# Performance work log

Measured on AMD Instinct MI355X. Metric: run time of the kernel, lower is better.

The kernel has to match this reference:

```python
import jax, jax.numpy as jnp
import numpy as np

B, S, E, H = 4, 1024, 256, 8
D = E // H


def setup_inputs() -> dict:
    key = jax.random.key(0)
    ks = jax.random.split(key, 10)
    def lin(k, fin, fout):
        return jax.random.normal(k, (fin, fout), jnp.float32) / np.sqrt(fin)
    return {
        'x': jax.random.normal(ks[0], (B, S, E), jnp.float32),
        'Wq': lin(ks[1], E, E),
        'Wk': lin(ks[2], E, E),
        'Wv': lin(ks[3], E, E),
        'W_off1': lin(ks[4], E, E // 2),
        'b_off1': jnp.zeros((E // 2,), jnp.float32),
        'W_off2': lin(ks[5], E // 2, 2 * H),
        'b_off2': jnp.zeros((2 * H,), jnp.float32),
        'W_out': lin(ks[6], E, E),
        'b_out': jnp.zeros((E,), jnp.float32),
    }


def _forward(x, Wq, Wk, Wv, W_off1, b_off1, W_off2, b_off2, W_out, b_out):
    Bb, Ss, Ee = x.shape
    scale = 1.0 / np.sqrt(D)
    # offsets: (B,S,H,2) -- [...,0]=x-offset (col), [...,1]=y-offset (row)
    off = jax.nn.gelu(x @ W_off1 + b_off1, approximate=False) @ W_off2 + b_off2
    off = off.reshape(Bb, Ss, H, 2)
    q = (x @ Wq).reshape(Bb, Ss, H, D).transpose(0, 2, 1, 3)  # bhsd
    k = (x @ Wk).reshape(Bb, Ss, H, D).transpose(0, 2, 1, 3)
    v = (x @ Wv).reshape(Bb, Ss, H, D).transpose(0, 2, 1, 3)
    scores = jnp.einsum('bhid,bhjd->bhij', q, k) * scale  # (B,H,S,S)

    ox = off[..., 0].transpose(0, 2, 1)  # (B,H,S)
    oy = off[..., 1].transpose(0, 2, 1)
    cols = jnp.arange(Ss, dtype=x.dtype)
    xs = cols[None, None, None, :] + ox[..., None]          # (B,H,S,S) sample col
    ys = cols[None, None, :, None] + oy[..., None]          # (B,H,S,1) sample row

    x0 = jnp.floor(xs); x1 = x0 + 1.0
    y0 = jnp.floor(ys); y1 = y0 + 1.0
    wx = xs - x0  # (B,H,S,S)
    wy = ys - y0  # (B,H,S,1)
    lim = jnp.asarray(Ss - 1, x.dtype)

    def corner(yf, xf):
        # bilinear corner sample with zeros padding (align_corners=True)
        yc = jnp.clip(yf, 0, lim).astype(jnp.int32)
        xc = jnp.clip(xf, 0, lim).astype(jnp.int32)
        rows = jnp.take_along_axis(scores, jnp.broadcast_to(yc, scores.shape), axis=2)
        vals = jnp.take_along_axis(rows, jnp.broadcast_to(xc, rows.shape), axis=3)
        valid = (yf >= 0) & (yf <= lim) & (xf >= 0) & (xf <= lim)
        return jnp.where(valid, vals, jnp.zeros((), x.dtype))

    deformed = (corner(y0, x0) * (1 - wy) * (1 - wx)
                + corner(y0, x1) * (1 - wy) * wx
                + corner(y1, x0) * wy * (1 - wx)
                + corner(y1, x1) * wy * wx)

    attn = jax.nn.softmax(deformed, axis=-1)  # dropout is identity in eval
    out = jnp.einsum('bhij,bhjd->bhid', attn, v)
    out = out.transpose(0, 2, 1, 3).reshape(Bb, Ss, Ee)
    return out @ W_out + b_out


def reference(x, Wq, Wk, Wv, W_off1, b_off1, W_off2, b_off2, W_out, b_out):
    return _forward(x, Wq, Wk, Wv, W_off1, b_off1, W_off2, b_off2, W_out, b_out)
```

## Files before the change

kernel.cpp:

```cpp
#include <hip/hip_runtime.h>

typedef unsigned short u16;
typedef __attribute__((ext_vector_type(8))) short short8;
typedef __attribute__((ext_vector_type(4))) float f32x4;

__device__ __forceinline__ float bf2f(u16 u) {
    union { unsigned int i; float f; } z;
    z.i = ((unsigned int)u) << 16;
    return z.f;
}
__device__ __forceinline__ u16 f2bf(float f) {
    union { float f; unsigned int i; } z;
    z.f = f;
    unsigned int i = z.i;
    return (u16)((i + 0x7fffu + ((i >> 16) & 1u)) >> 16);
}
__device__ __forceinline__ int sniff_bf16(const u16* __restrict__ x) {
    u16 u = x[threadIdx.x & 63];
    int e = (u >> 7) & 0xFF;
    bool sane = (e >= 110 && e <= 135) || (u == 0);
    unsigned long long m = __ballot(sane);
    return (__popcll(m) >= 50) ? 1 : 0;
}
__device__ __forceinline__ float cvt_elem(const void* p, int i, int fl) {
    return fl ? bf2f(((const u16*)p)[i]) : ((const float*)p)[i];
}

#define SB 1024
#define EB 256
#define NH 8
#define HD 32

__global__ __launch_bounds__(256) void k_prep(
    const void* x, const void* wq, const void* wk, const void* wv, const void* w1,
    const void* w2, const void* wo, const void* b1, const void* b2, const void* bo,
    u16* __restrict__ xb, u16* __restrict__ Wcat, u16* __restrict__ Wot,
    u16* __restrict__ W2t, float* __restrict__ b1f, float* __restrict__ b2f,
    float* __restrict__ bof) {
    __shared__ float tile[64][65];
    int fl = sniff_bf16((const u16*)x);
    int t = threadIdx.x;
    int bid = blockIdx.x;
    if (bid < 1024) {
        int idx = bid * 1024 + t * 4;
        if (fl) {
            *(ushort4*)(xb + idx) = *(const ushort4*)((const u16*)x + idx);
        } else {
            float4 v = *(const float4*)((const float*)x + idx);
            ushort4 s;
            s.x = f2bf(v.x); s.y = f2bf(v.y); s.z = f2bf(v.z); s.w = f2bf(v.w);
            *(ushort4*)(xb + idx) = s;
        }
    } else if (bid == 1024) {
        #pragma unroll
        for (int it = 0; it < 10; ++it) {
            int idx = it * 256 + t;
            if (idx < 2048) {
                int n = idx >> 7, kk = idx & 127;
                W2t[idx] = f2bf(cvt_elem(w2, kk * 16 + n, fl));
            }
            else if (idx < 2176)  b1f[idx - 2048] = cvt_elem(b1, idx - 2048, fl);
            else if (idx < 2192)  b2f[idx - 2176] = cvt_elem(b2, idx - 2176, fl);
            else if (idx < 2448)  bof[idx - 2192] = cvt_elem(bo, idx - 2192, fl);
        }
    } else {
        int rel = bid - 1025;
        int z = rel >> 4, rr = rel & 15;
        int k0 = (rr & 3) * 64, n0 = (rr >> 2) * 64;
        const void* src;
        u16* dst;
        int ncols;
        if (z == 0)      { src = wq; dst = Wcat;             ncols = 256; }
        else if (z == 1) { src = wk; dst = Wcat + 256 * 256; ncols = 256; }
        else if (z == 2) { src = wv; dst = Wcat + 512 * 256; ncols = 256; }
        else if (z == 3) { src = w1; dst = Wcat + 768 * 256; ncols = 128; }
        else             { src = wo; dst = Wot;              ncols = 256; }
        if (n0 >= ncols) return;
        int lr = t >> 6, lc = t & 63;
        #pragma unroll
        for (int it = 0; it < 16; ++it) {
            int r = it * 4 + lr;
            tile[r][lc] = cvt_elem(src, (k0 + r) * ncols + n0 + lc, fl);
        }
        __syncthreads();
        #pragma unroll
        for (int it = 0; it < 16; ++it) {
            int n = it * 4 + lr;
            dst[(size_t)(n0 + n) * 256 + k0 + lc] = f2bf(tile[lc][n]);
        }
    }
}

__global__ __launch_bounds__(256) void k_qkvh(
    const u16* __restrict__ xb, const u16* __restrict__ Wt, const float* __restrict__ b1f,
    u16* __restrict__ q, u16* __restrict__ k, u16* __restrict__ v, u16* __restrict__ hb) {
    int t = threadIdx.x;
    int w = t >> 6, L = t & 63;
    int lane15 = L & 15, quad = L >> 4;
    int Wid = blockIdx.x * 4 + w;
    int mtile = Wid & 127, ntile = Wid >> 7;
    int m0 = mtile * 32, n0 = ntile * 32;
    const u16* ap0 = xb + (size_t)(m0 + lane15) * 256 + quad * 8;
    const u16* ap1 = ap0 + 16 * 256;
    const u16* bp0 = Wt + (size_t)(n0 + lane15) * 256 + quad * 8;
    const u16* bp1 = bp0 + 16 * 256;
    bool vreg = (ntile >= 16 && ntile < 24);
    f32x4 acc[2][2];
    #pragma unroll
    for (int a = 0; a < 2; ++a)
        #pragma unroll
        for (int c = 0; c < 2; ++c) acc[a][c] = (f32x4){0.0f, 0.0f, 0.0f, 0.0f};
    if (!vreg) {
        #pragma unroll
        for (int kc = 0; kc < 256; kc += 32) {
            short8 a0 = *(const short8*)(ap0 + kc);
            short8 a1 = *(const short8*)(ap1 + kc);
            short8 b0 = *(const short8*)(bp0 + kc);
            short8 b1 = *(const short8*)(bp1 + kc);
            acc[0][0] = __builtin_amdgcn_mfma_f32_16x16x32_bf16(b0, a0, acc[0][0], 0, 0, 0);
            acc[0][1] = __builtin_amdgcn_mfma_f32_16x16x32_bf16(b1, a0, acc[0][1], 0, 0, 0);
            acc[1][0] = __builtin_amdgcn_mfma_f32_16x16x32_bf16(b0, a1, acc[1][0], 0, 0, 0);
            acc[1][1] = __builtin_amdgcn_mfma_f32_16x16x32_bf16(b1, a1, acc[1][1], 0, 0, 0);
        }
    } else {
        #pragma unroll
        for (int kc = 0; kc < 256; kc += 32) {
            short8 a0 = *(const short8*)(ap0 + kc);
            short8 a1 = *(const short8*)(ap1 + kc);
            short8 b0 = *(const short8*)(bp0 + kc);
            short8 b1 = *(const short8*)(bp1 + kc);
            acc[0][0] = __builtin_amdgcn_mfma_f32_16x16x32_bf16(a0, b0, acc[0][0], 0, 0, 0);
            acc[0][1] = __builtin_amdgcn_mfma_f32_16x16x32_bf16(a0, b1, acc[0][1], 0, 0, 0);
            acc[1][0] = __builtin_amdgcn_mfma_f32_16x16x32_bf16(a1, b0, acc[1][0], 0, 0, 0);
            acc[1][1] = __builtin_amdgcn_mfma_f32_16x16x32_bf16(a1, b1, acc[1][1], 0, 0, 0);
        }
    }
    if (ntile < 16) {
        u16* dst = (ntile < 8) ? q : k;
        int hh = ntile & 7;
        #pragma unroll
        for (int xt = 0; xt < 2; ++xt)
            #pragma unroll
            for (int wt = 0; wt < 2; ++wt) {
                int m = m0 + xt * 16 + lane15;
                int b = m >> 10, s = m & 1023;
                int d = wt * 16 + quad * 4;
                ushort4 st;
                st.x = f2bf(acc[xt][wt][0]); st.y = f2bf(acc[xt][wt][1]);
                st.z = f2bf(acc[xt][wt][2]); st.w = f2bf(acc[xt][wt][3]);
                *(ushort4*)(dst + (((size_t)(b * NH + hh)) * SB + s) * HD + d) = st;
            }
    } else if (vreg) {
        int nl = (ntile - 16) * 32;
        #pragma unroll
        for (int mt = 0; mt < 2; ++mt)
            #pragma unroll
            for (int nt = 0; nt < 2; ++nt) {
                int n = nl + nt * 16 + lane15;
                int hh = n >> 5, d = n & 31;
                int mbase = m0 + mt * 16 + quad * 4;
                int b = mbase >> 10, s0 = mbase & 1023;
                ushort4 st;
                st.x = f2bf(acc[mt][nt][0]); st.y = f2bf(acc[mt][nt][1]);
                st.z = f2bf(acc[mt][nt][2]); st.w = f2bf(acc[mt][nt][3]);
                *(ushort4*)(v + (b * NH + hh) * (SB * HD) + (s0 >> 3) * 256 + d * 8 + (s0 & 7)) = st;
            }
    } else {
        int nl = (ntile - 24) * 32;
        #pragma unroll
        for (int xt = 0; xt < 2; ++xt)
            #pragma unroll
            for (int wt = 0; wt < 2; ++wt) {
                int m = m0 + xt * 16 + lane15;
                int hn = nl + wt * 16 + quad * 4;
                ushort4 st;
                #pragma unroll
                for (int reg = 0; reg < 4; ++reg) {
                    float aa = acc[xt][wt][reg] + b1f[hn + reg];
                    float g = 0.5f * aa * (1.0f + erff(aa * 0.70710678118654752f));
                    ((u16*)&st)[reg] = f2bf(g);
                }
                *(ushort4*)(hb + (size_t)m * 128 + hn) = st;
            }
    }
}

#define TSTR 1064
#define BLEND4A(R)                                                    \
    _Pragma("unroll")                                                 \
    for (int jj = 0; jj < 4; ++jj) {                                  \
        float dd = wxm * A8[(R) + jj] + wx * A8[(R) + jj + 1];        \
        float ee = __expf(dd);                                        \
        dv[c * 4 + jj] = ee;                                          \
        ls += ee;                                                     \
    }

__global__ __launch_bounds__(256) void k_attn(
    const u16* __restrict__ q, const u16* __restrict__ kmat,
    const u16* __restrict__ hb, const u16* __restrict__ W2t,
    const float* __restrict__ b2f,
    const u16* __restrict__ vfrag, u16* __restrict__ attn) {
    __shared__ u16 tbuf[16][TSTR];
    __shared__ float invLs[16];
    float* red = (float*)&tbuf[0][0];
    int t = threadIdx.x;
    int w = t >> 6, L = t & 63;
    int lane15 = L & 15, quad = L >> 4;
    int bh = blockIdx.y, it0 = blockIdx.x * 16;
    int b = bh >> 3, h = bh & 7;
    int mg0 = b * SB + it0;
    const float scale = 0.17677669529663687f;
    const u16* vb = vfrag + bh * (SB * HD);
    int kc0 = w * 256;

    {
        int row = t >> 4, ii = t & 15;
        tbuf[row][ii] = 0;
        tbuf[row][1040 + ii] = 0;
    }

    float ox_row;
    {
        const u16* hrow = hb + (size_t)(mg0 + lane15) * 128 + quad * 8;
        const u16* wrow = W2t + (size_t)lane15 * 128 + quad * 8;
        f32x4 oacc = {0.0f, 0.0f, 0.0f, 0.0f};
        #pragma unroll
        for (int c = 0; c < 4; ++c) {
            short8 aw = *(const short8*)(wrow + c * 32);
            short8 bh8 = *(const short8*)(hrow + c * 32);
            oacc = __builtin_amdgcn_mfma_f32_16x16x32_bf16(aw, bh8, oacc, 0, 0, 0);
        }
        int h2 = h * 2;
        int qs = h2 >> 2;
        bool rlo = ((h2 & 3) == 0);
        float selx = rlo ? oacc[0] : oacc[2];
        float sely = rlo ? oacc[1] : oacc[3];
        ox_row = __shfl(selx, qs * 16 + lane15) + b2f[h2];
        float oy_row = __shfl(sely, qs * 16 + lane15) + b2f[h2 + 1];
        float ysf = (float)(it0 + lane15) + oy_row;
        float y0f = floorf(ysf);
        float wy = ysf - y0f;
        float y1f = y0f + 1.0f;
        float alA = scale * (1.0f - wy) * ((y0f >= 0.0f && y0f <= 1023.0f) ? 1.0f : 0.0f);
        float alB = scale * wy * ((y1f >= 0.0f && y1f <= 1023.0f) ? 1.0f : 0.0f);
        int yc0 = (int)fminf(fmaxf(y0f, 0.0f), 1023.0f);
        int yc1 = (int)fminf(fmaxf(y1f, 0.0f), 1023.0f);

        const u16* qb = q + (size_t)bh * SB * HD;
        short8 q0 = *(const short8*)(qb + yc0 * HD + quad * 8);
        short8 q1 = *(const short8*)(qb + yc1 * HD + quad * 8);
        union { short8 v; u16 a[8]; } afr;
        #pragma unroll
        for (int s = 0; s < 8; ++s)
            afr.a[s] = f2bf(alA * bf2f((u16)q0[s]) + alB * bf2f((u16)q1[s]));

        const u16* kb = kmat + (size_t)bh * SB * HD;
        #pragma unroll
        for (int nt = 0; nt < 16; ++nt) {
            short8 bk = *(const short8*)(kb + (size_t)(kc0 + nt * 16 + lane15) * HD + quad * 8);
            f32x4 z = {0.0f, 0.0f, 0.0f, 0.0f};
            f32x4 acc = __builtin_amdgcn_mfma_f32_16x16x32_bf16(bk, afr.v, z, 0, 0, 0);
            uint2 pk;
            pk.x = (unsigned)f2bf(acc[0]) | ((unsigned)f2bf(acc[1]) << 16);
            pk.y = (unsigned)f2bf(acc[2]) | ((unsigned)f2bf(acc[3]) << 16);
            *(uint2*)&tbuf[lane15][16 + kc0 + nt * 16 + quad * 4] = pk;
        }
    }

    short8 vpre[8];
    #pragma unroll
    for (int c = 0; c < 4; ++c) {
        int kc = kc0 + c * 32;
        const u16* bp = vb + ((kc >> 3) + quad) * (HD * 8);
        vpre[c * 2]     = *(const short8*)(bp + lane15 * 8);
        vpre[c * 2 + 1] = *(const short8*)(bp + (lane15 + 16) * 8);
    }
    __syncthreads();

    #pragma unroll
    for (int r = 0; r < 4; ++r) {
        int m = w * 4 + r;
        float oxm = __shfl(ox_row, m);
        float fxf = floorf(oxm);
        float wx = oxm - fxf, wxm = 1.0f - wx;
        fxf = fminf(fmaxf(fxf, -1028.0f), 1028.0f);
        int fx = (int)fxf;
        int qd = fx >> 2, rm = fx & 3;
        float dv[16];
        float ls = 0.0f;
        #pragma unroll
        for (int c = 0; c < 4; ++c) {
            int colbase = c * 256 + 4 * (qd + L);
            int rd = colbase < -16 ? -16 : (colbase > 1032 ? 1032 : colbase);
            const u16* rp = &tbuf[m][16 + rd];
            ushort4 lo = *(const ushort4*)rp;
            ushort4 hi = *(const ushort4*)(rp + 4);
            float A8[8];
            A8[0] = bf2f(lo.x); A8[1] = bf2f(lo.y); A8[2] = bf2f(lo.z); A8[3] = bf2f(lo.w);
            A8[4] = bf2f(hi.x); A8[5] = bf2f(hi.y); A8[6] = bf2f(hi.z); A8[7] = bf2f(hi.w);
            if (rm == 0) { BLEND4A(0) }
            else if (rm == 1) { BLEND4A(1) }
            else if (rm == 2) { BLEND4A(2) }
            else { BLEND4A(3) }
        }
        #pragma unroll
        for (int o = 1; o < 64; o <<= 1) ls += __shfl_xor(ls, o);
        #pragma unroll
        for (int c = 0; c < 4; ++c) {
            unsigned lo = (unsigned)f2bf(dv[c * 4 + 0]) | ((unsigned)f2bf(dv[c * 4 + 1]) << 16);
            unsigned hi = (unsigned)f2bf(dv[c * 4 + 2]) | ((unsigned)f2bf(dv[c * 4 + 3]) << 16);
            *(uint2*)&tbuf[m][16 + c * 256 + 4 * L] = make_uint2(lo, hi);
        }
        if (L == 0) invLs[m] = 1.0f / ls;
    }
    __syncthreads();

    f32x4 acc0 = {0.0f, 0.0f, 0.0f, 0.0f};
    f32x4 acc1 = {0.0f, 0.0f, 0.0f, 0.0f};
    #pragma unroll
    for (int c = 0; c < 4; ++c) {
        int kc = kc0 + c * 32;
        short8 a = *(const short8*)&tbuf[lane15][16 + kc + quad * 8];
        acc0 = __builtin_amdgcn_mfma_f32_16x16x32_bf16(a, vpre[c * 2], acc0, 0, 0, 0);
        acc1 = __builtin_amdgcn_mfma_f32_16x16x32_bf16(a, vpre[c * 2 + 1], acc1, 0, 0, 0);
    }
    #pragma unroll
    for (int c = 4; c < 8; ++c) {
        int kc = kc0 + c * 32;
        short8 a = *(const short8*)&tbuf[lane15][16 + kc + quad * 8];
        const u16* bp = vb + ((kc >> 3) + quad) * (HD * 8);
        short8 b0 = *(const short8*)(bp + lane15 * 8);
        short8 b1 = *(const short8*)(bp + (lane15 + 16) * 8);
        acc0 = __builtin_amdgcn_mfma_f32_16x16x32_bf16(a, b0, acc0, 0, 0, 0);
        acc1 = __builtin_amdgcn_mfma_f32_16x16x32_bf16(a, b1, acc1, 0, 0, 0);
    }
    __syncthreads();
    *(f32x4*)&red[(((size_t)w * 2 + 0) * 64 + L) * 4] = acc0;
    *(f32x4*)&red[(((size_t)w * 2 + 1) * 64 + L) * 4] = acc1;
    __syncthreads();
    {
        int row = t >> 4, col = t & 15;
        int lsrc = col + 16 * (row >> 2);
        int reg = row & 3;
        float s0 = red[((0 * 64 + lsrc)) * 4 + reg] + red[((2 * 64 + lsrc)) * 4 + reg]
                 + red[((4 * 64 + lsrc)) * 4 + reg] + red[((6 * 64 + lsrc)) * 4 + reg];
        float s1 = red[((1 * 64 + lsrc)) * 4 + reg] + red[((3 * 64 + lsrc)) * 4 + reg]
                 + red[((5 * 64 + lsrc)) * 4 + reg] + red[((7 * 64 + lsrc)) * 4 + reg];
        float il = invLs[row];
        size_t o = ((size_t)(b * SB + it0 + row)) * EB + h * HD;
        attn[o + col]      = f2bf(s0 * il);
        attn[o + 16 + col] = f2bf(s1 * il);
    }
}

__global__ __launch_bounds__(256) void k_out(
    const u16* __restrict__ a, const u16* __restrict__ Wot, const float* __restrict__ bof,
    const u16* __restrict__ xsniff, void* __restrict__ outp) {
    int fl = sniff_bf16(xsniff);
    int t = threadIdx.x;
    int w = t >> 6, L = t & 63;
    int lane15 = L & 15, quad = L >> 4;
    int Wid = blockIdx.x * 4 + w;
    int m0 = (Wid & 255) * 16, n0 = (Wid >> 8) * 32;
    const u16* ap  = a + (size_t)(m0 + lane15) * 256 + quad * 8;
    const u16* bp0 = Wot + (size_t)(n0 + lane15) * 256 + quad * 8;
    const u16* bp1 = bp0 + 16 * 256;
    f32x4 acc0 = {0.0f, 0.0f, 0.0f, 0.0f};
    f32x4 acc1 = {0.0f, 0.0f, 0.0f, 0.0f};
    #pragma unroll
    for (int kc = 0; kc < 256; kc += 32) {
        short8 av = *(const short8*)(ap + kc);
        short8 b0 = *(const short8*)(bp0 + kc);
        short8 b1 = *(const short8*)(bp1 + kc);
        acc0 = __builtin_amdgcn_mfma_f32_16x16x32_bf16(b0, av, acc0, 0, 0, 0);
        acc1 = __builtin_amdgcn_mfma_f32_16x16x32_bf16(b1, av, acc1, 0, 0, 0);
    }
    int m = m0 + lane15;
    #pragma unroll
    for (int wt = 0; wt < 2; ++wt) {
        const f32x4& ac = wt ? acc1 : acc0;
        int n = n0 + wt * 16 + quad * 4;
        float4 bz = *(const float4*)(bof + n);
        float v0 = ac[0] + bz.x, v1 = ac[1] + bz.y, v2 = ac[2] + bz.z, v3 = ac[3] + bz.w;
        if (fl) {
            ushort4 st;
            st.x = f2bf(v0); st.y = f2bf(v1); st.z = f2bf(v2); st.w = f2bf(v3);
            *(ushort4*)((u16*)outp + (size_t)m * 256 + n) = st;
        } else {
            *(float4*)((float*)outp + (size_t)m * 256 + n) = make_float4(v0, v1, v2, v3);
        }
    }
}

extern "C" void kernel_launch(void* const* d_in, const int* in_sizes, int n_in,
                              void* d_out, int out_size, void* d_ws, size_t ws_size,
                              hipStream_t stream) {
    char* ws = (char*)d_ws;
    u16*    xb   = (u16*)(ws);
    u16*    Wcat = (u16*)(ws + 2097152);
    u16*    Wot  = (u16*)(ws + 2555904);
    u16*    W2t  = (u16*)(ws + 2686976);
    float*  b1f  = (float*)(ws + 2691072);
    float*  b2f  = (float*)(ws + 2691584);
    float*  bof  = (float*)(ws + 2691648);
    u16*    q    = (u16*)(ws + 2692672);
    u16*    k    = (u16*)(ws + 4789824);
    u16*    v    = (u16*)(ws + 6886976);
    u16*    hb   = (u16*)(ws + 8984128);
    u16*    attn = (u16*)(ws + 10032704);

    hipLaunchKernelGGL(k_prep, dim3(1105), dim3(256), 0, stream,
                       d_in[0], d_in[1], d_in[2], d_in[3], d_in[4],
                       d_in[6], d_in[8], d_in[5], d_in[7], d_in[9],
                       xb, Wcat, Wot, W2t, b1f, b2f, bof);
    hipLaunchKernelGGL(k_qkvh, dim3(896), dim3(256), 0, stream, xb, Wcat, b1f, q, k, v, hb);
    hipLaunchKernelGGL(k_attn, dim3(64, 32), dim3(256), 0, stream, q, k, hb, W2t, b2f, v, attn);
    hipLaunchKernelGGL(k_out, dim3(512), dim3(256), 0, stream, attn, Wot, bof,
                       (const u16*)d_in[0], (u16*)d_out);
}
```

Measured before the change: 143.4 us.

## Fuse x bf16 conversion into QKV GEMM loads and prefetch all V fragments

Drops the separate pass in k_prep that converted x to a bf16 workspace copy. The QKV/offset GEMM now reads x directly and converts fp32 fragments to bf16 on the fly, which removes a full write and re-read of x. The cost is that each GEMM wave re-reads fp32 x (twice the bytes) and converts redundantly across the 28 n-tiles. Separately, the attention kernel now prefetches all eight V fragment pairs into registers before the barrier instead of four, at the cost of higher register pressure.

```diff
diff --git a/kernel.cpp b/kernel.cpp
--- a/kernel.cpp
+++ b/kernel.cpp
@@ -25,6 +25,16 @@
 __device__ __forceinline__ float cvt_elem(const void* p, int i, int fl) {
     return fl ? bf2f(((const u16*)p)[i]) : ((const float*)p)[i];
 }
+__device__ __forceinline__ short8 load_xfrag(const void* x, int fl, size_t off) {
+    if (fl) return *(const short8*)((const u16*)x + off);
+    const float* xf = (const float*)x + off;
+    float4 u0 = *(const float4*)xf;
+    float4 u1 = *(const float4*)(xf + 4);
+    union { short8 v; u16 a[8]; } r;
+    r.a[0] = f2bf(u0.x); r.a[1] = f2bf(u0.y); r.a[2] = f2bf(u0.z); r.a[3] = f2bf(u0.w);
+    r.a[4] = f2bf(u1.x); r.a[5] = f2bf(u1.y); r.a[6] = f2bf(u1.z); r.a[7] = f2bf(u1.w);
+    return r.v;
+}
 
 #define SB 1024
 #define EB 256
@@ -34,24 +44,14 @@
 __global__ __launch_bounds__(256) void k_prep(
     const void* x, const void* wq, const void* wk, const void* wv, const void* w1,
     const void* w2, const void* wo, const void* b1, const void* b2, const void* bo,
-    u16* __restrict__ xb, u16* __restrict__ Wcat, u16* __restrict__ Wot,
+    u16* __restrict__ Wcat, u16* __restrict__ Wot,
     u16* __restrict__ W2t, float* __restrict__ b1f, float* __restrict__ b2f,
     float* __restrict__ bof) {
     __shared__ float tile[64][65];
     int fl = sniff_bf16((const u16*)x);
     int t = threadIdx.x;
     int bid = blockIdx.x;
-    if (bid < 1024) {
-        int idx = bid * 1024 + t * 4;
-        if (fl) {
-            *(ushort4*)(xb + idx) = *(const ushort4*)((const u16*)x + idx);
-        } else {
-            float4 v = *(const float4*)((const float*)x + idx);
-            ushort4 s;
-            s.x = f2bf(v.x); s.y = f2bf(v.y); s.z = f2bf(v.z); s.w = f2bf(v.w);
-            *(ushort4*)(xb + idx) = s;
-        }
-    } else if (bid == 1024) {
+    if (bid == 0) {
         #pragma unroll
         for (int it = 0; it < 10; ++it) {
             int idx = it * 256 + t;
@@ -64,7 +64,7 @@
             else if (idx < 2448)  bof[idx - 2192] = cvt_elem(bo, idx - 2192, fl);
         }
     } else {
-        int rel = bid - 1025;
+        int rel = bid - 1;
         int z = rel >> 4, rr = rel & 15;
         int k0 = (rr & 3) * 64, n0 = (rr >> 2) * 64;
         const void* src;
@@ -92,16 +92,17 @@
 }
 
 __global__ __launch_bounds__(256) void k_qkvh(
-    const u16* __restrict__ xb, const u16* __restrict__ Wt, const float* __restrict__ b1f,
+    const void* __restrict__ x, const u16* __restrict__ Wt, const float* __restrict__ b1f,
     u16* __restrict__ q, u16* __restrict__ k, u16* __restrict__ v, u16* __restrict__ hb) {
+    int fl = sniff_bf16((const u16*)x);
     int t = threadIdx.x;
     int w = t >> 6, L = t & 63;
     int lane15 = L & 15, quad = L >> 4;
     int Wid = blockIdx.x * 4 + w;
     int mtile = Wid & 127, ntile = Wid >> 7;
     int m0 = mtile * 32, n0 = ntile * 32;
-    const u16* ap0 = xb + (size_t)(m0 + lane15) * 256 + quad * 8;
-    const u16* ap1 = ap0 + 16 * 256;
+    size_t aoff0 = (size_t)(m0 + lane15) * 256 + quad * 8;
+    size_t aoff1 = aoff0 + 16 * 256;
     const u16* bp0 = Wt + (size_t)(n0 + lane15) * 256 + quad * 8;
     const u16* bp1 = bp0 + 16 * 256;
     bool vreg = (ntile >= 16 && ntile < 24);
@@ -113,8 +114,8 @@
     if (!vreg) {
         #pragma unroll
         for (int kc = 0; kc < 256; kc += 32) {
-            short8 a0 = *(const short8*)(ap0 + kc);
-            short8 a1 = *(const short8*)(ap1 + kc);
+            short8 a0 = load_xfrag(x, fl, aoff0 + kc);
+            short8 a1 = load_xfrag(x, fl, aoff1 + kc);
             short8 b0 = *(const short8*)(bp0 + kc);
             short8 b1 = *(const short8*)(bp1 + kc);
             acc[0][0] = __builtin_amdgcn_mfma_f32_16x16x32_bf16(b0, a0, acc[0][0], 0, 0, 0);
@@ -125,8 +126,8 @@
     } else {
         #pragma unroll
         for (int kc = 0; kc < 256; kc += 32) {
-            short8 a0 = *(const short8*)(ap0 + kc);
-            short8 a1 = *(const short8*)(ap1 + kc);
+            short8 a0 = load_xfrag(x, fl, aoff0 + kc);
+            short8 a1 = load_xfrag(x, fl, aoff1 + kc);
             short8 b0 = *(const short8*)(bp0 + kc);
             short8 b1 = *(const short8*)(bp1 + kc);
             acc[0][0] = __builtin_amdgcn_mfma_f32_16x16x32_bf16(a0, b0, acc[0][0], 0, 0, 0);
@@ -267,13 +268,13 @@
         }
     }
 
-    short8 vpre[8];
-    #pragma unroll
-    for (int c = 0; c < 4; ++c) {
+    short8 vpre0[8], vpre1[8];
+    #pragma unroll
+    for (int c = 0; c < 8; ++c) {
         int kc = kc0 + c * 32;
         const u16* bp = vb + ((kc >> 3) + quad) * (HD * 8);
-        vpre[c * 2]     = *(const short8*)(bp + lane15 * 8);
-        vpre[c * 2 + 1] = *(const short8*)(bp + (lane15 + 16) * 8);
+        vpre0[c] = *(const short8*)(bp + lane15 * 8);
+        vpre1[c] = *(const short8*)(bp + (lane15 + 16) * 8);
     }
     __syncthreads();
 
@@ -318,21 +319,11 @@
     f32x4 acc0 = {0.0f, 0.0f, 0.0f, 0.0f};
     f32x4 acc1 = {0.0f, 0.0f, 0.0f, 0.0f};
     #pragma unroll
-    for (int c = 0; c < 4; ++c) {
+    for (int c = 0; c < 8; ++c) {
         int kc = kc0 + c * 32;
         short8 a = *(const short8*)&tbuf[lane15][16 + kc + quad * 8];
-        acc0 = __builtin_amdgcn_mfma_f32_16x16x32_bf16(a, vpre[c * 2], acc0, 0, 0, 0);
-        acc1 = __builtin_amdgcn_mfma_f32_16x16x32_bf16(a, vpre[c * 2 + 1], acc1, 0, 0, 0);
-    }
-    #pragma unroll
-    for (int c = 4; c < 8; ++c) {
-        int kc = kc0 + c * 32;
-        short8 a = *(const short8*)&tbuf[lane15][16 + kc + quad * 8];
-        const u16* bp = vb + ((kc >> 3) + quad) * (HD * 8);
-        short8 b0 = *(const short8*)(bp + lane15 * 8);
-        short8 b1 = *(const short8*)(bp + (lane15 + 16) * 8);
-        acc0 = __builtin_amdgcn_mfma_f32_16x16x32_bf16(a, b0, acc0, 0, 0, 0);
-        acc1 = __builtin_amdgcn_mfma_f32_16x16x32_bf16(a, b1, acc1, 0, 0, 0);
+        acc0 = __builtin_amdgcn_mfma_f32_16x16x32_bf16(a, vpre0[c], acc0, 0, 0, 0);
+        acc1 = __builtin_amdgcn_mfma_f32_16x16x32_bf16(a, vpre1[c], acc1, 0, 0, 0);
     }
     __syncthreads();
     *(f32x4*)&red[(((size_t)w * 2 + 0) * 64 + L) * 4] = acc0;
@@ -396,24 +387,23 @@
                               void* d_out, int out_size, void* d_ws, size_t ws_size,
                               hipStream_t stream) {
     char* ws = (char*)d_ws;
-    u16*    xb   = (u16*)(ws);
-    u16*    Wcat = (u16*)(ws + 2097152);
-    u16*    Wot  = (u16*)(ws + 2555904);
-    u16*    W2t  = (u16*)(ws + 2686976);
-    float*  b1f  = (float*)(ws + 2691072);
-    float*  b2f  = (float*)(ws + 2691584);
-    float*  bof  = (float*)(ws + 2691648);
-    u16*    q    = (u16*)(ws + 2692672);
-    u16*    k    = (u16*)(ws + 4789824);
-    u16*    v    = (u16*)(ws + 6886976);
-    u16*    hb   = (u16*)(ws + 8984128);
-    u16*    attn = (u16*)(ws + 10032704);
-
-    hipLaunchKernelGGL(k_prep, dim3(1105), dim3(256), 0, stream,
+    u16*    Wcat = (u16*)(ws);
+    u16*    Wot  = (u16*)(ws + 458752);
+    u16*    W2t  = (u16*)(ws + 589824);
+    float*  b1f  = (float*)(ws + 593920);
+    float*  b2f  = (float*)(ws + 594432);
+    float*  bof  = (float*)(ws + 594496);
+    u16*    q    = (u16*)(ws + 595520);
+    u16*    k    = (u16*)(ws + 2692672);
+    u16*    v    = (u16*)(ws + 4789824);
+    u16*    hb   = (u16*)(ws + 6886976);
+    u16*    attn = (u16*)(ws + 7935552);
+
+    hipLaunchKernelGGL(k_prep, dim3(81), dim3(256), 0, stream,
                        d_in[0], d_in[1], d_in[2], d_in[3], d_in[4],
                        d_in[6], d_in[8], d_in[5], d_in[7], d_in[9],
-                       xb, Wcat, Wot, W2t, b1f, b2f, bof);
-    hipLaunchKernelGGL(k_qkvh, dim3(896), dim3(256), 0, stream, xb, Wcat, b1f, q, k, v, hb);
+                       Wcat, Wot, W2t, b1f, b2f, bof);
+    hipLaunchKernelGGL(k_qkvh, dim3(896), dim3(256), 0, stream, d_in[0], Wcat, b1f, q, k, v, hb);
     hipLaunchKernelGGL(k_attn, dim3(64, 32), dim3(256), 0, stream, q, k, hb, W2t, b2f, v, attn);
     hipLaunchKernelGGL(k_out, dim3(512), dim3(256), 0, stream, attn, Wot, bof,
                        (const u16*)d_in[0], (u16*)d_out);
```

Result: slower. 150.3 us (+4.8%).
